# Performance work log

Measured on AMD Instinct MI355X. Metric: run time of the kernel, lower is better.

The kernel has to match this reference:

```python
import jax, jax.numpy as jnp
import numpy as np

B = 128      # graphs per batch
NPG = 40     # nodes per graph (<= MAXN)
N = B * NPG  # total nodes
E = 20000    # total edges
LP = 512     # protein sequence length
NPROT = 229  # KIBA proteins
MAXN = 45    # to_dense_batch max_num_nodes


def _gcn(x, W, b, src, dst, n):
    # PyG GCNConv: symmetric-normalized adjacency with self-loops.
    xw = x @ W
    deg = jnp.zeros((n,), xw.dtype).at[dst].add(1.0) + 1.0  # +1 for self-loop
    dinv = jax.lax.rsqrt(deg)
    msg = xw[src] * (dinv[src] * dinv[dst])[:, None]
    agg = jnp.zeros_like(xw).at[dst].add(msg) + xw * (1.0 / deg)[:, None]
    return agg + b


def _to_dense_batch(x, batch, num_graphs, max_nodes):
    n = x.shape[0]
    counts = jnp.zeros((num_graphs,), jnp.int32).at[batch].add(1)
    starts = jnp.concatenate([jnp.zeros((1,), jnp.int32), jnp.cumsum(counts)[:-1].astype(jnp.int32)])
    pos = jnp.arange(n, dtype=jnp.int32) - starts[batch]
    idx = batch * max_nodes + pos
    dense = jnp.zeros((num_graphs * max_nodes, x.shape[1]), x.dtype).at[idx].set(x)
    return dense.reshape(num_graphs, max_nodes, x.shape[1])


def setup_inputs() -> dict:
    key = jax.random.key(0)
    ks = jax.random.split(key, 32)
    xav = lambda k, s: jax.random.normal(k, s, jnp.float32) * jnp.sqrt(2.0 / (s[0] + s[-1]))
    x = jax.random.normal(ks[0], (N, 78), jnp.float32)
    src = jax.random.randint(ks[1], (E,), 0, N)
    dst = (src // NPG) * NPG + jax.random.randint(ks[2], (E,), 0, NPG)  # intra-graph edges
    edge_index = jnp.stack([src, dst]).astype(jnp.int32)
    target_id = jax.random.randint(ks[3], (B,), 0, NPROT).astype(jnp.int32)
    batch = (jnp.arange(N) // NPG).astype(jnp.int32)
    proteins = jax.random.normal(ks[4], (NPROT, LP, 1280), jnp.float32) * 0.1
    return dict(
        x=x, edge_index=edge_index, target_id=target_id, batch=batch, proteins=proteins,
        gW1=xav(ks[5], (78, 128)), gb1=jnp.zeros((128,), jnp.float32),
        gW2=xav(ks[6], (128, 128)), gb2=jnp.zeros((128,), jnp.float32),
        gW3=xav(ks[7], (128, 256)), gb3=jnp.zeros((256,), jnp.float32),
        fc1_W=xav(ks[8], (256, 1024)), fc1_b=jnp.zeros((1024,), jnp.float32),
        fc2_W=xav(ks[9], (1024, 128)), fc2_b=jnp.zeros((128,), jnp.float32),
        bert1_W=xav(ks[10], (1280, 128)), bert1_b=jnp.zeros((128,), jnp.float32),
        bert2_W=xav(ks[11], (128, 128)), bert2_b=jnp.zeros((128,), jnp.float32),
        W_b=xav(ks[12], (128, 128)), W_c=xav(ks[13], (32, 128)), W_p=xav(ks[14], (32, 128)),
        w_hc=xav(ks[15], (32, 1)), w_hp=xav(ks[16], (32, 1)),
        cat1_W=xav(ks[17], (256, 1024)), cat1_b=jnp.zeros((1024,), jnp.float32),
        cat2_W=xav(ks[18], (1024, 512)), cat2_b=jnp.zeros((512,), jnp.float32),
        out_W=xav(ks[19], (512, 1)), out_b=jnp.zeros((1,), jnp.float32),
    )


def _forward(x, proteins, gW1, gb1, gW2, gb2, gW3, gb3, fc1_W, fc1_b, fc2_W, fc2_b,
             bert1_W, bert1_b, bert2_W, bert2_b, W_b, W_c, W_p, w_hc, w_hp,
             cat1_W, cat1_b, cat2_W, cat2_b, out_W, out_b,
             edge_index, target_id, batch):
    relu, tanh = jax.nn.relu, jnp.tanh
    src, dst = edge_index[0], edge_index[1]
    # --- GCN stack (dropout is identity in eval) ---
    h = relu(_gcn(x, gW1, gb1, src, dst, x.shape[0]))
    h = relu(_gcn(h, gW2, gb2, src, dst, x.shape[0]))
    h = relu(_gcn(h, gW3, gb3, src, dst, x.shape[0]))  # [N, 256]
    hd = _to_dense_batch(h, batch, B, MAXN)            # [B, 45, 256]
    hd = relu(hd @ fc1_W + fc1_b)
    hd = relu(hd @ fc2_W + fc2_b)                      # [B, 45, 128]
    xc = jnp.transpose(hd, (0, 2, 1))                  # [B, 128, 45]
    # --- protein branch ---
    t = proteins[target_id]                            # [B, LP, 1280]
    t = relu(t @ bert1_W + bert1_b)
    t = relu(t @ bert2_W + bert2_b)                    # [B, LP, 128]
    # --- parallel co-attention ---
    C = tanh(jnp.einsum('blk,km,bms->bls', t, W_b, xc))       # [B, LP, 45]
    Wcx = jnp.einsum('km,bms->bks', W_c, xc)                  # [B, 32, 45]
    Wpt = jnp.einsum('km,blm->bkl', W_p, t)                   # [B, 32, LP]
    H_c = tanh(Wcx + jnp.einsum('bkl,bls->bks', Wpt, C))      # [B, 32, 45]
    H_p = tanh(Wpt + jnp.einsum('bks,bls->bkl', Wcx, C))      # [B, 32, LP]
    a_c = jax.nn.softmax(jnp.einsum('k,bks->bs', w_hc[:, 0], H_c), axis=-1)  # [B, 45]
    a_p = jax.nn.softmax(jnp.einsum('k,bkl->bl', w_hp[:, 0], H_p), axis=-1)  # [B, LP]
    c = jnp.einsum('bs,bms->bm', a_c, xc)                     # [B, 128]
    p = jnp.einsum('bl,blm->bm', a_p, t)                      # [B, 128]
    cp = jnp.concatenate([c, p], axis=1)                      # [B, 256]
    cp = relu(cp @ cat1_W + cat1_b)
    cp = relu(cp @ cat2_W + cat2_b)
    return cp @ out_W + out_b                                 # [B, 1]


def reference(x, edge_index, target_id, batch, proteins, gW1, gb1, gW2, gb2, gW3, gb3,
              fc1_W, fc1_b, fc2_W, fc2_b, bert1_W, bert1_b, bert2_W, bert2_b,
              W_b, W_c, W_p, w_hc, w_hp, cat1_W, cat1_b, cat2_W, cat2_b, out_W, out_b):
    return _forward(x, proteins, gW1, gb1, gW2, gb2, gW3, gb3, fc1_W, fc1_b, fc2_W, fc2_b,
                    bert1_W, bert1_b, bert2_W, bert2_b, W_b, W_c, W_p, w_hc, w_hp,
                    cat1_W, cat1_b, cat2_W, cat2_b, out_W, out_b,
                    edge_index, target_id, batch)
```

## Files before the change

kernel.cpp:

```cpp
#include <hip/hip_runtime.h>
#include <hip/hip_bf16.h>

typedef __hip_bfloat16 bf16;
typedef __bf16 bf16x8 __attribute__((ext_vector_type(8)));
typedef float f32x4 __attribute__((ext_vector_type(4)));

#define NB   128
#define NPGX 40
#define NNODE 5120
#define NE   20000
#define LPX  512
#define MAXNX 45
#define EMAX 512

__device__ __forceinline__ void stv(float* p, float v) { *p = v; }
__device__ __forceinline__ void stv(bf16* p, float v) { *p = __float2bfloat16(v); }
__device__ __forceinline__ ushort f2bf(float f) {
    uint x = __float_as_uint(f);
    return (ushort)((x + 0x7fffu + ((x >> 16) & 1u)) >> 16);
}
__device__ __forceinline__ float bf2f(ushort u) { return __uint_as_float(((uint)u) << 16); }
__device__ __forceinline__ float dot4(f32x4 a, f32x4 b) {
    return a[0]*b[0] + a[1]*b[1] + a[2]*b[2] + a[3]*b[3];
}

template <typename TA, typename TO, int ACT, bool GATHER>
__global__ __launch_bounds__(256) void gemm_mfma(
    const TA* __restrict__ A, const ushort* __restrict__ BT, const float* __restrict__ bias,
    TO* __restrict__ C, int M, int N, int K, const int* __restrict__ tgt)
{
    __shared__ __align__(16) ushort sA[128][40];
    __shared__ __align__(16) ushort sB[128][40];
    const int t = threadIdx.x;
    const int lane = t & 63;
    const int wave = t >> 6;
    const int wr = wave >> 1, wc = wave & 1;
    const int m0 = blockIdx.x * 128;
    const int n0 = blockIdx.y * 128;
    const int fr = lane & 15;
    const int kh = lane >> 4;

    f32x4 acc[4][4] = {};

    for (int k0 = 0; k0 < K; k0 += 32) {
        if constexpr (sizeof(TA) == 2) {
            const ushort* Ap = (const ushort*)A;
#pragma unroll
            for (int i = 0; i < 2; i++) {
                int linear = i * 2048 + t * 8;
                int row = linear >> 5, k = linear & 31;
                long gr = m0 + row;
                uint4 v = *(const uint4*)(Ap + gr * (long)K + k0 + k);
                *(uint4*)&sA[row][k] = v;
            }
        } else {
            const float* Ap = (const float*)A;
#pragma unroll
            for (int i = 0; i < 4; i++) {
                int linear = i * 1024 + t * 4;
                int row = linear >> 5, k = linear & 31;
                long gr = m0 + row;
                if (GATHER) { int bb = (int)(gr >> 9); gr = (long)tgt[bb] * LPX + (gr & 511); }
                float4 v = *(const float4*)(Ap + gr * (long)K + k0 + k);
                ushort4 h;
                h.x = f2bf(v.x); h.y = f2bf(v.y); h.z = f2bf(v.z); h.w = f2bf(v.w);
                *(ushort4*)&sA[row][k] = h;
            }
        }
#pragma unroll
        for (int i = 0; i < 2; i++) {
            int linear = i * 2048 + t * 8;
            int row = linear >> 5, k = linear & 31;
            uint4 v = *(const uint4*)(BT + (long)(n0 + row) * K + k0 + k);
            *(uint4*)&sB[row][k] = v;
        }
        __syncthreads();

        bf16x8 a[4], b[4];
#pragma unroll
        for (int mf = 0; mf < 4; mf++)
            a[mf] = *(const bf16x8*)&sA[wr * 64 + mf * 16 + fr][kh * 8];
#pragma unroll
        for (int nf = 0; nf < 4; nf++)
            b[nf] = *(const bf16x8*)&sB[wc * 64 + nf * 16 + fr][kh * 8];
#pragma unroll
        for (int mf = 0; mf < 4; mf++)
#pragma unroll
            for (int nf = 0; nf < 4; nf++)
                acc[mf][nf] = __builtin_amdgcn_mfma_f32_16x16x32_bf16(a[mf], b[nf], acc[mf][nf], 0, 0, 0);
        __syncthreads();
    }

#pragma unroll
    for (int mf = 0; mf < 4; mf++) {
#pragma unroll
        for (int nf = 0; nf < 4; nf++) {
            int coln = n0 + wc * 64 + nf * 16 + fr;
            float bv = bias ? bias[coln] : 0.f;
#pragma unroll
            for (int r = 0; r < 4; r++) {
                int row = m0 + wr * 64 + mf * 16 + kh * 4 + r;
                float v = acc[mf][nf][r] + bv;
                if (ACT == 1) v = fmaxf(v, 0.f);
                else if (ACT == 2) v = tanhf(v);
                stv(&C[(long)row * N + coln], v);
            }
        }
    }
}

__global__ __launch_bounds__(256) void gemm_mfma64(
    const ushort* __restrict__ A, const ushort* __restrict__ BT, const float* __restrict__ bias,
    float* __restrict__ C, int M, int N, int K)
{
    __shared__ __align__(16) ushort sA[64][40];
    __shared__ __align__(16) ushort sB[64][40];
    const int t = threadIdx.x;
    const int lane = t & 63;
    const int wave = t >> 6;
    const int wr = wave >> 1, wc = wave & 1;
    const int m0 = blockIdx.x * 64;
    const int n0 = blockIdx.y * 64;
    const int fr = lane & 15;
    const int kh = lane >> 4;

    f32x4 acc[2][2] = {};

    for (int k0 = 0; k0 < K; k0 += 32) {
        {
            int linear = t * 8;
            int row = linear >> 5, k = linear & 31;
            *(uint4*)&sA[row][k] = *(const uint4*)(A + (long)(m0 + row) * K + k0 + k);
            *(uint4*)&sB[row][k] = *(const uint4*)(BT + (long)(n0 + row) * K + k0 + k);
        }
        __syncthreads();
        bf16x8 a[2], b[2];
#pragma unroll
        for (int mf = 0; mf < 2; mf++)
            a[mf] = *(const bf16x8*)&sA[wr * 32 + mf * 16 + fr][kh * 8];
#pragma unroll
        for (int nf = 0; nf < 2; nf++)
            b[nf] = *(const bf16x8*)&sB[wc * 32 + nf * 16 + fr][kh * 8];
#pragma unroll
        for (int mf = 0; mf < 2; mf++)
#pragma unroll
            for (int nf = 0; nf < 2; nf++)
                acc[mf][nf] = __builtin_amdgcn_mfma_f32_16x16x32_bf16(a[mf], b[nf], acc[mf][nf], 0, 0, 0);
        __syncthreads();
    }

#pragma unroll
    for (int mf = 0; mf < 2; mf++) {
#pragma unroll
        for (int nf = 0; nf < 2; nf++) {
            int coln = n0 + wc * 32 + nf * 16 + fr;
            float bv = bias[coln];
#pragma unroll
            for (int r = 0; r < 4; r++) {
                int row = m0 + wr * 32 + mf * 16 + kh * 4 + r;
                C[(long)row * N + coln] = fmaxf(acc[mf][nf][r] + bv, 0.f);
            }
        }
    }
}

__device__ __forceinline__ void gcn_gemm(const float (*hin)[132], float (*hout)[260],
                                         float (*sW)[260], const float* __restrict__ Wg,
                                         int K, int N, int NQ, int t) {
    f32x4 acc[10] = {};
    for (int k0 = 0; k0 < K; k0 += 32) {
        int kmax = min(32, K - k0);
        int kpad = (kmax + 3) & ~3;
        __syncthreads();
        for (int o = t; o < kpad * N; o += 256) {
            int row = o / N, c = o - row * N;
            sW[row][c] = (row < kmax) ? Wg[(k0 + row) * N + c] : 0.f;
        }
        __syncthreads();
        for (int kk = 0; kk < kpad; kk += 4) {
#pragma unroll 10
            for (int j = 0; j < NQ; j++) {
                int q = t + j * 256;
                int i = q / (N / 4), f = (q % (N / 4)) * 4;
                f32x4 hv = *(const f32x4*)&hin[i][k0 + kk];
#pragma unroll
                for (int d = 0; d < 4; d++) {
                    f32x4 wv = *(const f32x4*)&sW[kk + d][f];
                    acc[j][0] = fmaf(hv[d], wv[0], acc[j][0]);
                    acc[j][1] = fmaf(hv[d], wv[1], acc[j][1]);
                    acc[j][2] = fmaf(hv[d], wv[2], acc[j][2]);
                    acc[j][3] = fmaf(hv[d], wv[3], acc[j][3]);
                }
            }
        }
    }
    __syncthreads();
#pragma unroll 10
    for (int j = 0; j < NQ; j++) {
        int q = t + j * 256;
        int i = q / (N / 4), f = (q % (N / 4)) * 4;
        *(f32x4*)&hout[i][f] = acc[j];
    }
}

__device__ __forceinline__ void gcn_agg(const float (*hout)[260], float (*hin)[132],
                                        const float* __restrict__ bias,
                                        const float* __restrict__ dgi,
                                        const int* __restrict__ rs,
                                        const int* __restrict__ colv,
                                        const float* __restrict__ valv,
                                        float* __restrict__ hd, int N, bool tohd, int g, int t) {
    for (int o = t; o < 40 * N; o += 256) {
        int i = o / N, f = o - i * N;
        float s = hout[i][f] * dgi[i];
        int e0 = rs[i], e1 = rs[i + 1];
        for (int e = e0; e < e1; e++) s += valv[e] * hout[colv[e]][f];
        s += bias[f];
        s = fmaxf(s, 0.f);
        if (tohd) hd[(g * MAXNX + i) * N + f] = s;
        else      hin[i][f] = s;
    }
    if (tohd) for (int o = t; o < 5 * N; o += 256) hd[(g * MAXNX + 40) * N + o] = 0.f;
}

__global__ __launch_bounds__(256) void k_prep(
    const float* __restrict__ x, const int* __restrict__ ei,
    const float* __restrict__ W1, const float* __restrict__ b1,
    const float* __restrict__ W2, const float* __restrict__ b2,
    const float* __restrict__ W3, const float* __restrict__ b3,
    float* __restrict__ hd,
    const float* __restrict__ ws0, const float* __restrict__ ws1,
    const float* __restrict__ ws2, const float* __restrict__ ws3,
    ushort* __restrict__ wd0, ushort* __restrict__ wd1,
    ushort* __restrict__ wd2, ushort* __restrict__ wd3)
{
    __shared__ __align__(16) float hin[40][132];
    __shared__ __align__(16) float hout[40][260];
    __shared__ __align__(16) float sW[32][260];
    __shared__ int   s_cnt[40], s_cur[40], s_rs[41];
    __shared__ int   s_col[EMAX];
    __shared__ float s_val[EMAX];
    __shared__ float s_dinv[40], s_dgi[40];

    const int t = threadIdx.x;

    if (blockIdx.x >= NB) {
        float (*ts)[33] = reinterpret_cast<float(*)[33]>(&hin[0][0]);
        int bid = blockIdx.x - NB;
        const float* in; ushort* out; int K, N, b;
        if (bid < 256)      { in = ws0; out = wd0; K = 256;  N = 1024; b = bid; }
        else if (bid < 384) { in = ws1; out = wd1; K = 1024; N = 128;  b = bid - 256; }
        else if (bid < 544) { in = ws2; out = wd2; K = 1280; N = 128;  b = bid - 384; }
        else                { in = ws3; out = wd3; K = 128;  N = 128;  b = bid - 544; }
        int ktiles = K / 32;
        int kt = (b % ktiles) * 32, nt = (b / ktiles) * 32;
        int tn = t & 31, tk = t >> 5;
#pragma unroll
        for (int i = 0; i < 4; i++)
            ts[tk + i * 8][tn] = in[(long)(kt + tk + i * 8) * N + nt + tn];
        __syncthreads();
#pragma unroll
        for (int i = 0; i < 4; i++)
            out[(long)(nt + tk + i * 8) * K + kt + tn] = f2bf(ts[tn][tk + i * 8]);
        return;
    }

    const int g = blockIdx.x;
    const int base = g * NPGX;
    const int* srcp = ei;
    const int* dstp = ei + NE;

    for (int o = t; o < 40; o += 256) { s_cnt[o] = 0; s_cur[o] = 0; }
    for (int o = t; o < 40 * 78; o += 256) hin[o / 78][o % 78] = x[base * 78 + o];
    for (int o = t; o < 80; o += 256) hin[o >> 1][78 + (o & 1)] = 0.f;
    __syncthreads();
    for (int e = t; e < NE; e += 256) {
        int dl = dstp[e] - base;
        if ((unsigned)dl < 40u) atomicAdd(&s_cnt[dl], 1);
    }
    __syncthreads();
    if (t == 0) {
        int acc = 0;
        for (int i = 0; i < 40; i++) { s_rs[i] = acc; acc += s_cnt[i]; }
        s_rs[40] = acc;
    }
    if (t < 40) {
        float deg = (float)(s_cnt[t] + 1);
        s_dinv[t] = rsqrtf(deg);
        s_dgi[t] = 1.f / deg;
    }
    __syncthreads();
    for (int e = t; e < NE; e += 256) {
        int dl = dstp[e] - base;
        if ((unsigned)dl < 40u) {
            int sl = srcp[e] - base;
            int p = atomicAdd(&s_cur[dl], 1);
            int idx = s_rs[dl] + p;
            if (idx < EMAX) { s_col[idx] = sl; s_val[idx] = s_dinv[sl] * s_dinv[dl]; }
        }
    }
    __syncthreads();

    gcn_gemm(hin, hout, sW, W1, 78, 128, 5, t);
    __syncthreads();
    gcn_agg(hout, hin, b1, s_dgi, s_rs, s_col, s_val, nullptr, 128, false, g, t);
    __syncthreads();
    gcn_gemm(hin, hout, sW, W2, 128, 128, 5, t);
    __syncthreads();
    gcn_agg(hout, hin, b2, s_dgi, s_rs, s_col, s_val, nullptr, 128, false, g, t);
    __syncthreads();
    gcn_gemm(hin, hout, sW, W3, 128, 256, 10, t);
    __syncthreads();
    gcn_agg(hout, nullptr, b3, s_dgi, s_rs, s_col, s_val, hd, 256, true, g, t);
}

__global__ __launch_bounds__(512) void k_coatt_head(
    const ushort* __restrict__ t2, const float* __restrict__ hd2,
    const float* __restrict__ W_b, const float* __restrict__ W_c,
    const float* __restrict__ W_p, const float* __restrict__ w_hc,
    const float* __restrict__ w_hp,
    const float* __restrict__ cat1_W, const float* __restrict__ cat1_b,
    const float* __restrict__ cat2_W, const float* __restrict__ cat2_b,
    const float* __restrict__ outW, const float* __restrict__ outb,
    float* __restrict__ out)
{
    __shared__ __align__(16) float  sx[48][132];
    __shared__ __align__(16) ushort sY[48][136];
    __shared__ __align__(16) ushort sWpb[32][136];
    __shared__ __align__(16) float  sWcx[32][48];
    __shared__ __align__(16) float  sHc[32][48];
    __shared__ __align__(16) ushort sT[128][136];
    __shared__ __align__(16) float  sC[128][52];
    __shared__ __align__(16) float  sWpt[32][132];
    __shared__ float  sLogit[512];
    __shared__ float  sLc[64];
    __shared__ float  swh[64];
    __shared__ float  sRed[8], sRed2[8];
    __shared__ float  sPc[4][128];
    __shared__ float  sCin[256];

    const int b = blockIdx.x, tid = threadIdx.x;
    const int lane = tid & 63, wave = tid >> 6;
    const int fr = lane & 15, kh = lane >> 4;

    for (int o = tid; o < 48 * 32; o += 512) {
        int r = o >> 5, q = (o & 31) * 4;
        f32x4 v = {0.f, 0.f, 0.f, 0.f};
        if (r < 45) v = *(const f32x4*)&hd2[(b * 45 + r) * 128 + q];
        *(f32x4*)&sx[r][q] = v;
    }
    for (int o = tid; o < 32 * 32; o += 512) {
        int r = o >> 5, q = (o & 31) * 4;
        f32x4 v = *(const f32x4*)&W_p[r * 128 + q];
        sWpb[r][q] = f2bf(v[0]); sWpb[r][q + 1] = f2bf(v[1]);
        sWpb[r][q + 2] = f2bf(v[2]); sWpb[r][q + 3] = f2bf(v[3]);
    }
    if (tid < 64) swh[tid] = (tid < 32) ? w_hc[tid] : w_hp[tid - 32];
    for (int o = tid; o < 32 * 12; o += 512) {
        int r = o / 12, q = (o - r * 12) * 4;
        *(f32x4*)&sHc[r][q] = f32x4{0.f, 0.f, 0.f, 0.f};
    }
    __syncthreads();

    {
        int kg = tid >> 3, sg = tid & 7;
        float acc[12] = {};
        for (int m = 0; m < 128; m += 4) {
            f32x4 w0 = *(const f32x4*)&W_b[(2 * kg) * 128 + m];
            f32x4 w1 = *(const f32x4*)&W_b[(2 * kg + 1) * 128 + m];
#pragma unroll
            for (int u = 0; u < 6; u++) {
                f32x4 xv = *(const f32x4*)&sx[6 * sg + u][m];
                acc[u] += dot4(w0, xv);
                acc[6 + u] += dot4(w1, xv);
            }
        }
#pragma unroll
        for (int u = 0; u < 6; u++) {
            int s = 6 * sg + u;
            sY[s][2 * kg] = f2bf(acc[u]);
            sY[s][2 * kg + 1] = f2bf(acc[6 + u]);
        }
    }
    if (tid < 256) {
        int k = tid >> 3, sg = tid & 7;
        float acc[6] = {};
        for (int m = 0; m < 128; m += 4) {
            f32x4 w = *(const f32x4*)&W_c[k * 128 + m];
#pragma unroll
            for (int u = 0; u < 6; u++) {
                f32x4 xv = *(const f32x4*)&sx[6 * sg + u][m];
                acc[u] += dot4(w, xv);
            }
        }
#pragma unroll
        for (int u = 0; u < 6; u++) sWcx[k][6 * sg + u] = acc[u];
    }
    __syncthreads();

    const ushort* t2b = t2 + ((size_t)b * 512) * 128;

    for (int lc = 0; lc < 4; lc++) {
        {
            const ushort* srcp = t2b + lc * 128 * 128;
#pragma unroll
            for (int i = 0; i < 4; i++) {
                int idx = tid + i * 512;
                int row = idx >> 4, c8 = (idx & 15) * 8;
                *(uint4*)&sT[row][c8] = *(const uint4*)(srcp + row * 128 + c8);
            }
        }
        __syncthreads();
        {
            f32x4 cacc[3] = {};
            f32x4 wacc[2] = {};
#pragma unroll
            for (int ks = 0; ks < 4; ks++) {
                bf16x8 af = *(const bf16x8*)&sT[wave * 16 + fr][ks * 32 + kh * 8];
#pragma unroll
                for (int nt = 0; nt < 3; nt++) {
                    bf16x8 bf = *(const bf16x8*)&sY[nt * 16 + fr][ks * 32 + kh * 8];
                    cacc[nt] = __builtin_amdgcn_mfma_f32_16x16x32_bf16(af, bf, cacc[nt], 0, 0, 0);
                }
#pragma unroll
                for (int mt = 0; mt < 2; mt++) {
                    bf16x8 aw = *(const bf16x8*)&sWpb[mt * 16 + fr][ks * 32 + kh * 8];
                    wacc[mt] = __builtin_amdgcn_mfma_f32_16x16x32_bf16(aw, af, wacc[mt], 0, 0, 0);
                }
            }
#pragma unroll
            for (int nt = 0; nt < 3; nt++)
#pragma unroll
                for (int r = 0; r < 4; r++)
                    sC[wave * 16 + kh * 4 + r][nt * 16 + fr] = tanhf(cacc[nt][r]);
#pragma unroll
            for (int mt = 0; mt < 2; mt++)
#pragma unroll
                for (int r = 0; r < 4; r++)
                    sWpt[mt * 16 + kh * 4 + r][wave * 16 + fr] = wacc[mt][r];
        }
        __syncthreads();
        float hpacc[8];
        {
            if (tid < 384) {
                int k = tid / 12, sg = tid - (tid / 12) * 12;
                f32x4 a = {0.f, 0.f, 0.f, 0.f};
                for (int l = 0; l < 128; l++) {
                    float wv = sWpt[k][l];
                    f32x4 cv = *(const f32x4*)&sC[l][sg * 4];
                    a[0] = fmaf(wv, cv[0], a[0]); a[1] = fmaf(wv, cv[1], a[1]);
                    a[2] = fmaf(wv, cv[2], a[2]); a[3] = fmaf(wv, cv[3], a[3]);
                }
                f32x4 h = *(const f32x4*)&sHc[k][sg * 4];
                h[0] += a[0]; h[1] += a[1]; h[2] += a[2]; h[3] += a[3];
                *(f32x4*)&sHc[k][sg * 4] = h;
            }
            int kg = tid >> 5, li = tid & 31;
            float acc[8] = {};
            for (int s4 = 0; s4 < 48; s4 += 4) {
                f32x4 w0 = *(const f32x4*)&sWcx[2 * kg][s4];
                f32x4 w1 = *(const f32x4*)&sWcx[2 * kg + 1][s4];
#pragma unroll
                for (int u = 0; u < 4; u++) {
                    f32x4 cv = *(const f32x4*)&sC[li + 32 * u][s4];
                    acc[u] += dot4(w0, cv);
                    acc[4 + u] += dot4(w1, cv);
                }
            }
#pragma unroll
            for (int u = 0; u < 8; u++) hpacc[u] = acc[u];
        }
        __syncthreads();
        {
            int kg = tid >> 5, li = tid & 31;
#pragma unroll
            for (int u = 0; u < 4; u++) {
                sWpt[2 * kg][li + 32 * u] = tanhf(sWpt[2 * kg][li + 32 * u] + hpacc[u]);
                sWpt[2 * kg + 1][li + 32 * u] = tanhf(sWpt[2 * kg + 1][li + 32 * u] + hpacc[4 + u]);
            }
        }
        __syncthreads();
        if (tid < 128) {
            float a = 0.f;
            for (int k = 0; k < 32; k++) a += swh[32 + k] * sWpt[k][tid];
            sLogit[lc * 128 + tid] = a;
        }
        __syncthreads();
    }

    {
        int k = tid >> 4, si = tid & 15;
        sHc[k][si] = tanhf(sWcx[k][si] + sHc[k][si]);
        sHc[k][si + 16] = tanhf(sWcx[k][si + 16] + sHc[k][si + 16]);
        sHc[k][si + 32] = tanhf(sWcx[k][si + 32] + sHc[k][si + 32]);
    }
    __syncthreads();
    if (tid < 45) {
        float a = 0.f;
        for (int k = 0; k < 32; k++) a += swh[k] * sHc[k][tid];
        sLc[tid] = a;
    }
    __syncthreads();
    if (tid < 64) {
        float v = (tid < 45) ? sLc[tid] : -1e30f;
        float mx = v;
        for (int off = 32; off; off >>= 1) mx = fmaxf(mx, __shfl_xor(mx, off));
        float e = (tid < 45) ? expf(v - mx) : 0.f;
        float sm = e;
        for (int off = 32; off; off >>= 1) sm += __shfl_xor(sm, off);
        if (tid < 45) sLc[tid] = e / sm;
    }
    __syncthreads();
    if (tid < 128) {
        float c = 0.f;
        for (int s = 0; s < 45; s++) c += sLc[s] * sx[s][tid];
        sCin[tid] = c;
    }
    {
        float v = sLogit[tid];
        float mx = v;
        for (int off = 32; off; off >>= 1) mx = fmaxf(mx, __shfl_xor(mx, off));
        if ((tid & 63) == 0) sRed[tid >> 6] = mx;
        __syncthreads();
        mx = sRed[0];
#pragma unroll
        for (int w = 1; w < 8; w++) mx = fmaxf(mx, sRed[w]);
        float e = expf(v - mx);
        float sm = e;
        for (int off = 32; off; off >>= 1) sm += __shfl_xor(sm, off);
        if ((tid & 63) == 0) sRed2[tid >> 6] = sm;
        __syncthreads();
        sm = 0.f;
#pragma unroll
        for (int w = 0; w < 8; w++) sm += sRed2[w];
        sLogit[tid] = e / sm;
    }
    __syncthreads();
    {
        int gq = tid >> 7, m = tid & 127;
        float pp = 0.f;
        for (int l = gq * 128; l < gq * 128 + 128; l++)
            pp += sLogit[l] * bf2f(t2b[l * 128 + m]);
        sPc[gq][m] = pp;
    }
    __syncthreads();
    if (tid < 128)
        sCin[128 + tid] = sPc[0][tid] + sPc[1][tid] + sPc[2][tid] + sPc[3][tid];
    __syncthreads();

    float* sH1 = (float*)&sT[0][0];
    float* sH2 = sH1 + 1024;
#pragma unroll
    for (int j = 0; j < 2; j++) {
        int n = tid + j * 512;
        float a = cat1_b[n];
        for (int k = 0; k < 256; k++) a = fmaf(sCin[k], cat1_W[k * 1024 + n], a);
        sH1[n] = fmaxf(a, 0.f);
    }
    __syncthreads();
    {
        float a = cat2_b[tid];
        for (int k = 0; k < 1024; k++) a = fmaf(sH1[k], cat2_W[k * 512 + tid], a);
        sH2[tid] = fmaxf(a, 0.f);
    }
    __syncthreads();
    {
        float a = sH2[tid] * outW[tid];
        for (int off = 32; off; off >>= 1) a += __shfl_xor(a, off);
        if ((tid & 63) == 0) sRed[tid >> 6] = a;
        __syncthreads();
        if (tid == 0) {
            float s = 0.f;
#pragma unroll
            for (int w = 0; w < 8; w++) s += sRed[w];
            out[b] = s + outb[0];
        }
    }
}

extern "C" void kernel_launch(void* const* d_in, const int* in_sizes, int n_in,
                              void* d_out, int out_size, void* d_ws, size_t ws_size,
                              hipStream_t stream) {
    const float* x        = (const float*)d_in[0];
    const int*   ei       = (const int*)d_in[1];
    const int*   tgt      = (const int*)d_in[2];
    const float* proteins = (const float*)d_in[4];
    const float* gW1 = (const float*)d_in[5];  const float* gb1 = (const float*)d_in[6];
    const float* gW2 = (const float*)d_in[7];  const float* gb2 = (const float*)d_in[8];
    const float* gW3 = (const float*)d_in[9];  const float* gb3 = (const float*)d_in[10];
    const float* fc1_W = (const float*)d_in[11]; const float* fc1_b = (const float*)d_in[12];
    const float* fc2_W = (const float*)d_in[13]; const float* fc2_b = (const float*)d_in[14];
    const float* bert1_W = (const float*)d_in[15]; const float* bert1_b = (const float*)d_in[16];
    const float* bert2_W = (const float*)d_in[17]; const float* bert2_b = (const float*)d_in[18];
    const float* W_b = (const float*)d_in[19];
    const float* W_c = (const float*)d_in[20];
    const float* W_p = (const float*)d_in[21];
    const float* w_hc = (const float*)d_in[22];
    const float* w_hp = (const float*)d_in[23];
    const float* cat1_W = (const float*)d_in[24]; const float* cat1_b = (const float*)d_in[25];
    const float* cat2_W = (const float*)d_in[26]; const float* cat2_b = (const float*)d_in[27];
    const float* out_W = (const float*)d_in[28]; const float* out_b = (const float*)d_in[29];

    char* w = (char*)d_ws;
    auto alloc = [&](size_t bytes) -> void* {
        void* p = (void*)w;
        w += (bytes + 255) & ~(size_t)255;
        return p;
    };
    float* hd        = (float*)alloc((size_t)5760 * 256 * 4);
    bf16*  fc1o      = (bf16*)alloc((size_t)5760 * 1024 * 2);
    float* hd2       = (float*)alloc((size_t)5760 * 128 * 4);
    bf16*  t1        = (bf16*)alloc((size_t)65536 * 128 * 2);
    bf16*  t2        = (bf16*)alloc((size_t)65536 * 128 * 2);
    ushort* fc1_WT   = (ushort*)alloc((size_t)1024 * 256 * 2);
    ushort* fc2_WT   = (ushort*)alloc((size_t)128 * 1024 * 2);
    ushort* bert1_WT = (ushort*)alloc((size_t)128 * 1280 * 2);
    ushort* bert2_WT = (ushort*)alloc((size_t)128 * 128 * 2);

    k_prep<<<NB + 560, 256, 0, stream>>>(x, ei, gW1, gb1, gW2, gb2, gW3, gb3, hd,
                                         fc1_W, fc2_W, bert1_W, bert2_W,
                                         fc1_WT, fc2_WT, bert1_WT, bert2_WT);
    gemm_mfma<float, bf16, 1, false><<<dim3(45, 8), 256, 0, stream>>>(hd, fc1_WT, fc1_b, fc1o, 5760, 1024, 256, nullptr);
    gemm_mfma64<<<dim3(90, 2), 256, 0, stream>>>((const ushort*)fc1o, fc2_WT, fc2_b, hd2, 5760, 128, 1024);
    gemm_mfma<float, bf16, 1, true><<<dim3(512, 1), 256, 0, stream>>>(proteins, bert1_WT, bert1_b, t1, 65536, 128, 1280, tgt);
    gemm_mfma<ushort, bf16, 1, false><<<dim3(512, 1), 256, 0, stream>>>((const ushort*)t1, bert2_WT, bert2_b, t2, 65536, 128, 128, nullptr);
    k_coatt_head<<<NB, 512, 0, stream>>>((const ushort*)t2, hd2, W_b, W_c, W_p, w_hc, w_hp,
                                         cat1_W, cat1_b, cat2_W, cat2_b, out_W, out_b,
                                         (float*)d_out);
}
```

Measured before the change: 1.165 ms.

## Fuse bert1+bert2 GEMMs, merge fc1 into same launch, move fc2 into head

The two protein MLP GEMMs are fused into one kernel, and the bert1 output tile stays in shared memory as bf16 for the second GEMM, so the t1 intermediate never goes to global memory. The fc1 GEMM runs as extra blocks of the same launch, and the fc2 GEMM moves into the co-attention head kernel, one graph per block. This cuts the launch count from six to three and removes a global round trip for t1 and hd2. The cost is more serialized work inside each head block (a 1024-deep fc2 GEMM per graph over only 128 blocks) and some extra vectorized shared-memory reads in an inner loop.

New measurement: 1.152 ms. About the same (-1.1%).

```diff
diff --git a/kernel.cpp b/kernel.cpp
--- a/kernel.cpp
+++ b/kernel.cpp
@@ -13,8 +13,6 @@
 #define MAXNX 45
 #define EMAX 512
 
-__device__ __forceinline__ void stv(float* p, float v) { *p = v; }
-__device__ __forceinline__ void stv(bf16* p, float v) { *p = __float2bfloat16(v); }
 __device__ __forceinline__ ushort f2bf(float f) {
     uint x = __float_as_uint(f);
     return (ushort)((x + 0x7fffu + ((x >> 16) & 1u)) >> 16);
@@ -22,146 +20,6 @@
 __device__ __forceinline__ float bf2f(ushort u) { return __uint_as_float(((uint)u) << 16); }
 __device__ __forceinline__ float dot4(f32x4 a, f32x4 b) {
     return a[0]*b[0] + a[1]*b[1] + a[2]*b[2] + a[3]*b[3];
-}
-
-template <typename TA, typename TO, int ACT, bool GATHER>
-__global__ __launch_bounds__(256) void gemm_mfma(
-    const TA* __restrict__ A, const ushort* __restrict__ BT, const float* __restrict__ bias,
-    TO* __restrict__ C, int M, int N, int K, const int* __restrict__ tgt)
-{
-    __shared__ __align__(16) ushort sA[128][40];
-    __shared__ __align__(16) ushort sB[128][40];
-    const int t = threadIdx.x;
-    const int lane = t & 63;
-    const int wave = t >> 6;
-    const int wr = wave >> 1, wc = wave & 1;
-    const int m0 = blockIdx.x * 128;
-    const int n0 = blockIdx.y * 128;
-    const int fr = lane & 15;
-    const int kh = lane >> 4;
-
-    f32x4 acc[4][4] = {};
-
-    for (int k0 = 0; k0 < K; k0 += 32) {
-        if constexpr (sizeof(TA) == 2) {
-            const ushort* Ap = (const ushort*)A;
-#pragma unroll
-            for (int i = 0; i < 2; i++) {
-                int linear = i * 2048 + t * 8;
-                int row = linear >> 5, k = linear & 31;
-                long gr = m0 + row;
-                uint4 v = *(const uint4*)(Ap + gr * (long)K + k0 + k);
-                *(uint4*)&sA[row][k] = v;
-            }
-        } else {
-            const float* Ap = (const float*)A;
-#pragma unroll
-            for (int i = 0; i < 4; i++) {
-                int linear = i * 1024 + t * 4;
-                int row = linear >> 5, k = linear & 31;
-                long gr = m0 + row;
-                if (GATHER) { int bb = (int)(gr >> 9); gr = (long)tgt[bb] * LPX + (gr & 511); }
-                float4 v = *(const float4*)(Ap + gr * (long)K + k0 + k);
-                ushort4 h;
-                h.x = f2bf(v.x); h.y = f2bf(v.y); h.z = f2bf(v.z); h.w = f2bf(v.w);
-                *(ushort4*)&sA[row][k] = h;
-            }
-        }
-#pragma unroll
-        for (int i = 0; i < 2; i++) {
-            int linear = i * 2048 + t * 8;
-            int row = linear >> 5, k = linear & 31;
-            uint4 v = *(const uint4*)(BT + (long)(n0 + row) * K + k0 + k);
-            *(uint4*)&sB[row][k] = v;
-        }
-        __syncthreads();
-
-        bf16x8 a[4], b[4];
-#pragma unroll
-        for (int mf = 0; mf < 4; mf++)
-            a[mf] = *(const bf16x8*)&sA[wr * 64 + mf * 16 + fr][kh * 8];
-#pragma unroll
-        for (int nf = 0; nf < 4; nf++)
-            b[nf] = *(const bf16x8*)&sB[wc * 64 + nf * 16 + fr][kh * 8];
-#pragma unroll
-        for (int mf = 0; mf < 4; mf++)
-#pragma unroll
-            for (int nf = 0; nf < 4; nf++)
-                acc[mf][nf] = __builtin_amdgcn_mfma_f32_16x16x32_bf16(a[mf], b[nf], acc[mf][nf], 0, 0, 0);
-        __syncthreads();
-    }
-
-#pragma unroll
-    for (int mf = 0; mf < 4; mf++) {
-#pragma unroll
-        for (int nf = 0; nf < 4; nf++) {
-            int coln = n0 + wc * 64 + nf * 16 + fr;
-            float bv = bias ? bias[coln] : 0.f;
-#pragma unroll
-            for (int r = 0; r < 4; r++) {
-                int row = m0 + wr * 64 + mf * 16 + kh * 4 + r;
-                float v = acc[mf][nf][r] + bv;
-                if (ACT == 1) v = fmaxf(v, 0.f);
-                else if (ACT == 2) v = tanhf(v);
-                stv(&C[(long)row * N + coln], v);
-            }
-        }
-    }
-}
-
-__global__ __launch_bounds__(256) void gemm_mfma64(
-    const ushort* __restrict__ A, const ushort* __restrict__ BT, const float* __restrict__ bias,
-    float* __restrict__ C, int M, int N, int K)
-{
-    __shared__ __align__(16) ushort sA[64][40];
-    __shared__ __align__(16) ushort sB[64][40];
-    const int t = threadIdx.x;
-    const int lane = t & 63;
-    const int wave = t >> 6;
-    const int wr = wave >> 1, wc = wave & 1;
-    const int m0 = blockIdx.x * 64;
-    const int n0 = blockIdx.y * 64;
-    const int fr = lane & 15;
-    const int kh = lane >> 4;
-
-    f32x4 acc[2][2] = {};
-
-    for (int k0 = 0; k0 < K; k0 += 32) {
-        {
-            int linear = t * 8;
-            int row = linear >> 5, k = linear & 31;
-            *(uint4*)&sA[row][k] = *(const uint4*)(A + (long)(m0 + row) * K + k0 + k);
-            *(uint4*)&sB[row][k] = *(const uint4*)(BT + (long)(n0 + row) * K + k0 + k);
-        }
-        __syncthreads();
-        bf16x8 a[2], b[2];
-#pragma unroll
-        for (int mf = 0; mf < 2; mf++)
-            a[mf] = *(const bf16x8*)&sA[wr * 32 + mf * 16 + fr][kh * 8];
-#pragma unroll
-        for (int nf = 0; nf < 2; nf++)
-            b[nf] = *(const bf16x8*)&sB[wc * 32 + nf * 16 + fr][kh * 8];
-#pragma unroll
-        for (int mf = 0; mf < 2; mf++)
-#pragma unroll
-            for (int nf = 0; nf < 2; nf++)
-                acc[mf][nf] = __builtin_amdgcn_mfma_f32_16x16x32_bf16(a[mf], b[nf], acc[mf][nf], 0, 0, 0);
-        __syncthreads();
-    }
-
-#pragma unroll
-    for (int mf = 0; mf < 2; mf++) {
-#pragma unroll
-        for (int nf = 0; nf < 2; nf++) {
-            int coln = n0 + wc * 32 + nf * 16 + fr;
-            float bv = bias[coln];
-#pragma unroll
-            for (int r = 0; r < 4; r++) {
-                int row = m0 + wr * 32 + mf * 16 + kh * 4 + r;
-                C[(long)row * N + coln] = fmaxf(acc[mf][nf][r] + bv, 0.f);
-            }
-        }
-    }
 }
 
 __device__ __forceinline__ void gcn_gemm(const float (*hin)[132], float (*hout)[260],
@@ -223,7 +81,7 @@
     if (tohd) for (int o = t; o < 5 * N; o += 256) hd[(g * MAXNX + 40) * N + o] = 0.f;
 }
 
-__global__ __launch_bounds__(256) void k_prep(
+__global__ __launch_bounds__(256) void k_gcn_tr(
     const float* __restrict__ x, const int* __restrict__ ei,
     const float* __restrict__ W1, const float* __restrict__ b1,
     const float* __restrict__ W2, const float* __restrict__ b2,
@@ -314,8 +172,162 @@
     gcn_agg(hout, nullptr, b3, s_dgi, s_rs, s_col, s_val, hd, 256, true, g, t);
 }
 
+__global__ __launch_bounds__(256) void k_main(
+    const float* __restrict__ proteins, const int* __restrict__ tgt,
+    const ushort* __restrict__ bert1_WT, const float* __restrict__ bert1_b,
+    const ushort* __restrict__ bert2_WT, const float* __restrict__ bert2_b,
+    const float* __restrict__ hd, const ushort* __restrict__ fc1_WT,
+    const float* __restrict__ fc1_b,
+    ushort* __restrict__ t2, ushort* __restrict__ fc1o)
+{
+    __shared__ __align__(16) char smem[45056];
+    ushort (*uA)[40]   = (ushort(*)[40])smem;
+    ushort (*uT1)[136] = (ushort(*)[136])smem;
+    ushort (*uB)[40]   = (ushort(*)[40])(smem + 34816);
+
+    const int t = threadIdx.x;
+    const int lane = t & 63, wave = t >> 6;
+    const int wr = wave >> 1, wc = wave & 1;
+    const int fr = lane & 15, kh = lane >> 4;
+
+    if (blockIdx.x < 512) {
+        const int m0 = blockIdx.x * 128;
+        f32x4 acc[4][4] = {};
+        for (int k0 = 0; k0 < 1280; k0 += 32) {
+#pragma unroll
+            for (int i = 0; i < 4; i++) {
+                int linear = i * 1024 + t * 4;
+                int row = linear >> 5, k = linear & 31;
+                long gr = m0 + row;
+                int bb = (int)(gr >> 9); gr = (long)tgt[bb] * LPX + (gr & 511);
+                float4 v = *(const float4*)(proteins + gr * 1280L + k0 + k);
+                ushort4 h;
+                h.x = f2bf(v.x); h.y = f2bf(v.y); h.z = f2bf(v.z); h.w = f2bf(v.w);
+                *(ushort4*)&uA[row][k] = h;
+            }
+#pragma unroll
+            for (int i = 0; i < 2; i++) {
+                int linear = i * 2048 + t * 8;
+                int row = linear >> 5, k = linear & 31;
+                *(uint4*)&uB[row][k] = *(const uint4*)(bert1_WT + (long)row * 1280 + k0 + k);
+            }
+            __syncthreads();
+            bf16x8 a[4], b[4];
+#pragma unroll
+            for (int mf = 0; mf < 4; mf++)
+                a[mf] = *(const bf16x8*)&uA[wr * 64 + mf * 16 + fr][kh * 8];
+#pragma unroll
+            for (int nf = 0; nf < 4; nf++)
+                b[nf] = *(const bf16x8*)&uB[wc * 64 + nf * 16 + fr][kh * 8];
+#pragma unroll
+            for (int mf = 0; mf < 4; mf++)
+#pragma unroll
+                for (int nf = 0; nf < 4; nf++)
+                    acc[mf][nf] = __builtin_amdgcn_mfma_f32_16x16x32_bf16(a[mf], b[nf], acc[mf][nf], 0, 0, 0);
+            __syncthreads();
+        }
+#pragma unroll
+        for (int mf = 0; mf < 4; mf++)
+#pragma unroll
+            for (int nf = 0; nf < 4; nf++) {
+                int col = wc * 64 + nf * 16 + fr;
+                float bv = bert1_b[col];
+#pragma unroll
+                for (int r = 0; r < 4; r++) {
+                    int row = wr * 64 + mf * 16 + kh * 4 + r;
+                    uT1[row][col] = f2bf(fmaxf(acc[mf][nf][r] + bv, 0.f));
+                }
+            }
+        __syncthreads();
+        f32x4 acc2[4][4] = {};
+        for (int ks = 0; ks < 4; ks++) {
+#pragma unroll
+            for (int j = 0; j < 2; j++) {
+                int i2 = t + j * 256;
+                int row = i2 >> 2, q = (i2 & 3) * 8;
+                *(uint4*)&uB[row][q] = *(const uint4*)(bert2_WT + (long)row * 128 + ks * 32 + q);
+            }
+            __syncthreads();
+            bf16x8 a[4], b[4];
+#pragma unroll
+            for (int mf = 0; mf < 4; mf++)
+                a[mf] = *(const bf16x8*)&uT1[wr * 64 + mf * 16 + fr][ks * 32 + kh * 8];
+#pragma unroll
+            for (int nf = 0; nf < 4; nf++)
+                b[nf] = *(const bf16x8*)&uB[wc * 64 + nf * 16 + fr][kh * 8];
+#pragma unroll
+            for (int mf = 0; mf < 4; mf++)
+#pragma unroll
+                for (int nf = 0; nf < 4; nf++)
+                    acc2[mf][nf] = __builtin_amdgcn_mfma_f32_16x16x32_bf16(a[mf], b[nf], acc2[mf][nf], 0, 0, 0);
+            __syncthreads();
+        }
+#pragma unroll
+        for (int mf = 0; mf < 4; mf++)
+#pragma unroll
+            for (int nf = 0; nf < 4; nf++) {
+                int col = wc * 64 + nf * 16 + fr;
+                float bv = bert2_b[col];
+#pragma unroll
+                for (int r = 0; r < 4; r++) {
+                    int row = m0 + wr * 64 + mf * 16 + kh * 4 + r;
+                    t2[(long)row * 128 + col] = f2bf(fmaxf(acc2[mf][nf][r] + bv, 0.f));
+                }
+            }
+    } else {
+        int ft = blockIdx.x - 512;
+        const int m0 = (ft % 45) * 128;
+        const int n0 = (ft / 45) * 128;
+        f32x4 acc[4][4] = {};
+        for (int k0 = 0; k0 < 256; k0 += 32) {
+#pragma unroll
+            for (int i = 0; i < 4; i++) {
+                int linear = i * 1024 + t * 4;
+                int row = linear >> 5, k = linear & 31;
+                float4 v = *(const float4*)(hd + (long)(m0 + row) * 256 + k0 + k);
+                ushort4 h;
+                h.x = f2bf(v.x); h.y = f2bf(v.y); h.z = f2bf(v.z); h.w = f2bf(v.w);
+                *(ushort4*)&uA[row][k] = h;
+            }
+#pragma unroll
+            for (int i = 0; i < 2; i++) {
+                int linear = i * 2048 + t * 8;
+                int row = linear >> 5, k = linear & 31;
+                *(uint4*)&uB[row][k] = *(const uint4*)(fc1_WT + (long)(n0 + row) * 256 + k0 + k);
+            }
+            __syncthreads();
+            bf16x8 a[4], b[4];
+#pragma unroll
+            for (int mf = 0; mf < 4; mf++)
+                a[mf] = *(const bf16x8*)&uA[wr * 64 + mf * 16 + fr][kh * 8];
+#pragma unroll
+            for (int nf = 0; nf < 4; nf++)
+                b[nf] = *(const bf16x8*)&uB[wc * 64 + nf * 16 + fr][kh * 8];
+#pragma unroll
+            for (int mf = 0; mf < 4; mf++)
+#pragma unroll
+                for (int nf = 0; nf < 4; nf++)
+                    acc[mf][nf] = __builtin_amdgcn_mfma_f32_16x16x32_bf16(a[mf], b[nf], acc[mf][nf], 0, 0, 0);
+            __syncthreads();
+        }
+#pragma unroll
+        for (int mf = 0; mf < 4; mf++)
+#pragma unroll
+            for (int nf = 0; nf < 4; nf++) {
+                int col = n0 + wc * 64 + nf * 16 + fr;
+                float bv = fc1_b[col];
+#pragma unroll
+                for (int r = 0; r < 4; r++) {
+                    int row = m0 + wr * 64 + mf * 16 + kh * 4 + r;
+                    fc1o[(long)row * 1024 + col] = f2bf(fmaxf(acc[mf][nf][r] + bv, 0.f));
+                }
+            }
+    }
+}
+
 __global__ __launch_bounds__(512) void k_coatt_head(
-    const ushort* __restrict__ t2, const float* __restrict__ hd2,
+    const ushort* __restrict__ t2, const ushort* __restrict__ fc1o,
+    const ushort* __restrict__ fc2_WT, const float* __restrict__ fc2_b,
     const float* __restrict__ W_b, const float* __restrict__ W_c,
     const float* __restrict__ W_p, const float* __restrict__ w_hc,
     const float* __restrict__ w_hp,
@@ -343,12 +355,6 @@
     const int lane = tid & 63, wave = tid >> 6;
     const int fr = lane & 15, kh = lane >> 4;
 
-    for (int o = tid; o < 48 * 32; o += 512) {
-        int r = o >> 5, q = (o & 31) * 4;
-        f32x4 v = {0.f, 0.f, 0.f, 0.f};
-        if (r < 45) v = *(const f32x4*)&hd2[(b * 45 + r) * 128 + q];
-        *(f32x4*)&sx[r][q] = v;
-    }
     for (int o = tid; o < 32 * 32; o += 512) {
         int r = o >> 5, q = (o & 31) * 4;
         f32x4 v = *(const f32x4*)&W_p[r * 128 + q];
@@ -359,6 +365,44 @@
     for (int o = tid; o < 32 * 12; o += 512) {
         int r = o / 12, q = (o - r * 12) * 4;
         *(f32x4*)&sHc[r][q] = f32x4{0.f, 0.f, 0.f, 0.f};
+    }
+    if (tid < 96) {
+        int r = 45 + tid / 32, q = (tid & 31) * 4;
+        *(f32x4*)&sx[r][q] = f32x4{0.f, 0.f, 0.f, 0.f};
+    }
+
+    {
+        ushort (*sA2)[40] = (ushort(*)[40])&sT[0][0];
+        ushort (*sB2)[40] = (ushort(*)[40])((char*)&sT[0][0] + 4096);
+        f32x4 acc2[3] = {};
+        for (int k0 = 0; k0 < 1024; k0 += 32) {
+            if (tid < 192) {
+                int row = tid >> 2, q = (tid & 3) * 8;
+                *(uint4*)&sA2[row][q] = *(const uint4*)(fc1o + (size_t)(b * 45 + row) * 1024 + k0 + q);
+            }
+            {
+                int row = tid >> 2, q = (tid & 3) * 8;
+                *(uint4*)&sB2[row][q] = *(const uint4*)(fc2_WT + (size_t)row * 1024 + k0 + q);
+            }
+            __syncthreads();
+            bf16x8 bfr = *(const bf16x8*)&sB2[wave * 16 + fr][kh * 8];
+#pragma unroll
+            for (int mf = 0; mf < 3; mf++) {
+                bf16x8 afr = *(const bf16x8*)&sA2[mf * 16 + fr][kh * 8];
+                acc2[mf] = __builtin_amdgcn_mfma_f32_16x16x32_bf16(afr, bfr, acc2[mf], 0, 0, 0);
+            }
+            __syncthreads();
+        }
+#pragma unroll
+        for (int mf = 0; mf < 3; mf++) {
+            int col = wave * 16 + fr;
+            float bv = fc2_b[col];
+#pragma unroll
+            for (int r = 0; r < 4; r++) {
+                int row = mf * 16 + kh * 4 + r;
+                if (row < 45) sx[row][col] = fmaxf(acc2[mf][r] + bv, 0.f);
+            }
+        }
     }
     __syncthreads();
 
@@ -445,11 +489,14 @@
             if (tid < 384) {
                 int k = tid / 12, sg = tid - (tid / 12) * 12;
                 f32x4 a = {0.f, 0.f, 0.f, 0.f};
-                for (int l = 0; l < 128; l++) {
-                    float wv = sWpt[k][l];
-                    f32x4 cv = *(const f32x4*)&sC[l][sg * 4];
-                    a[0] = fmaf(wv, cv[0], a[0]); a[1] = fmaf(wv, cv[1], a[1]);
-                    a[2] = fmaf(wv, cv[2], a[2]); a[3] = fmaf(wv, cv[3], a[3]);
+                for (int l4 = 0; l4 < 128; l4 += 4) {
+                    f32x4 wv4 = *(const f32x4*)&sWpt[k][l4];
+#pragma unroll
+                    for (int d = 0; d < 4; d++) {
+                        f32x4 cv = *(const f32x4*)&sC[l4 + d][sg * 4];
+                        a[0] = fmaf(wv4[d], cv[0], a[0]); a[1] = fmaf(wv4[d], cv[1], a[1]);
+                        a[2] = fmaf(wv4[d], cv[2], a[2]); a[3] = fmaf(wv4[d], cv[3], a[3]);
+                    }
                 }
                 f32x4 h = *(const f32x4*)&sHc[k][sg * 4];
                 h[0] += a[0]; h[1] += a[1]; h[2] += a[2]; h[3] += a[3];
@@ -607,24 +654,21 @@
         w += (bytes + 255) & ~(size_t)255;
         return p;
     };
-    float* hd        = (float*)alloc((size_t)5760 * 256 * 4);
-    bf16*  fc1o      = (bf16*)alloc((size_t)5760 * 1024 * 2);
-    float* hd2       = (float*)alloc((size_t)5760 * 128 * 4);
-    bf16*  t1        = (bf16*)alloc((size_t)65536 * 128 * 2);
-    bf16*  t2        = (bf16*)alloc((size_t)65536 * 128 * 2);
-    ushort* fc1_WT   = (ushort*)alloc((size_t)1024 * 256 * 2);
-    ushort* fc2_WT   = (ushort*)alloc((size_t)128 * 1024 * 2);
-    ushort* bert1_WT = (ushort*)alloc((size_t)128 * 1280 * 2);
-    ushort* bert2_WT = (ushort*)alloc((size_t)128 * 128 * 2);
-
-    k_prep<<<NB + 560, 256, 0, stream>>>(x, ei, gW1, gb1, gW2, gb2, gW3, gb3, hd,
-                                         fc1_W, fc2_W, bert1_W, bert2_W,
-                                         fc1_WT, fc2_WT, bert1_WT, bert2_WT);
-    gemm_mfma<float, bf16, 1, false><<<dim3(45, 8), 256, 0, stream>>>(hd, fc1_WT, fc1_b, fc1o, 5760, 1024, 256, nullptr);
-    gemm_mfma64<<<dim3(90, 2), 256, 0, stream>>>((const ushort*)fc1o, fc2_WT, fc2_b, hd2, 5760, 128, 1024);
-    gemm_mfma<float, bf16, 1, true><<<dim3(512, 1), 256, 0, stream>>>(proteins, bert1_WT, bert1_b, t1, 65536, 128, 1280, tgt);
-    gemm_mfma<ushort, bf16, 1, false><<<dim3(512, 1), 256, 0, stream>>>((const ushort*)t1, bert2_WT, bert2_b, t2, 65536, 128, 128, nullptr);
-    k_coatt_head<<<NB, 512, 0, stream>>>((const ushort*)t2, hd2, W_b, W_c, W_p, w_hc, w_hp,
-                                         cat1_W, cat1_b, cat2_W, cat2_b, out_W, out_b,
-                                         (float*)d_out);
-}
+    float*  hd        = (float*)alloc((size_t)5760 * 256 * 4);
+    ushort* fc1o      = (ushort*)alloc((size_t)5760 * 1024 * 2);
+    ushort* t2        = (ushort*)alloc((size_t)65536 * 128 * 2);
+    ushort* fc1_WT    = (ushort*)alloc((size_t)1024 * 256 * 2);
+    ushort* fc2_WT    = (ushort*)alloc((size_t)128 * 1024 * 2);
+    ushort* bert1_WT  = (ushort*)alloc((size_t)128 * 1280 * 2);
+    ushort* bert2_WT  = (ushort*)alloc((size_t)128 * 128 * 2);
+
+    k_gcn_tr<<<NB + 560, 256, 0, stream>>>(x, ei, gW1, gb1, gW2, gb2, gW3, gb3, hd,
+                                           fc1_W, fc2_W, bert1_W, bert2_W,
+                                           fc1_WT, fc2_WT, bert1_WT, bert2_WT);
+    k_main<<<872, 256, 0, stream>>>(proteins, tgt, bert1_WT, bert1_b, bert2_WT, bert2_b,
+                                    hd, fc1_WT, fc1_b, t2, fc1o);
+    k_coatt_head<<<NB, 512, 0, stream>>>(t2, fc1o, fc2_WT, fc2_b,
+                                         W_b, W_c, W_p, w_hc, w_hp,
+                                         cat1_W, cat1_b, cat2_W, cat2_b,
+                                         out_W, out_b, (float*)d_out);
+}
```
